# Performance work log

Hardware: AMD Instinct MI355X
Metric: run time of the kernel (lower is better)

Reference implementation:

```python
import jax, jax.numpy as jnp
import numpy as np

E = 1024
B = 16
SV = 576
SL = 448


def setup_inputs() -> dict:
    key = jax.random.key(0)
    k1, k2, k3, k4, k5 = jax.random.split(key, 5)
    return {
        "vision_tokens": jax.random.normal(k1, (B, SV, E), dtype=jnp.float32),
        "language_tokens": jax.random.normal(k2, (B, SL, E), dtype=jnp.float32),
        "Wv": jax.random.normal(k3, (E, E), dtype=jnp.float32) * 0.02,  # vision_proj.weight
        "Wl": jax.random.normal(k4, (E, E), dtype=jnp.float32) * 0.02,  # language_proj.weight
        "Wo": jax.random.normal(k5, (E, E), dtype=jnp.float32) * 0.02,  # out_proj.weight
        "bo": jnp.zeros((E,), dtype=jnp.float32),                        # out_proj.bias
    }


def reference(vision_tokens, language_tokens, Wv, Wl, Wo, bo):
    # Separate modality projections (nn.Linear, no bias): y = x @ W.T
    vp = jnp.einsum("bsd,ed->bse", vision_tokens, Wv)
    lp = jnp.einsum("bsd,ed->bse", language_tokens, Wl)
    # Concat vision+language tokens along sequence dim
    x = jnp.concatenate([vp, lp], axis=1)  # [B, SV+SL, E]
    scale = x.shape[-1] ** -0.5  # 1/sqrt(embed_dim), single-head as in CPU path
    scores = jnp.einsum("bqe,bke->bqk", x, x) * scale
    attn = jax.nn.softmax(scores, axis=-1)
    attended = jnp.einsum("bqk,bke->bqe", attn, x)
    # out_proj (with bias)
    return jnp.einsum("bse,fe->bsf", attended, Wo) + bo
```

## Files before the change

kernel.cpp:

```cpp
#include <hip/hip_runtime.h>

typedef _Float16 f16;
typedef _Float16 f16x4 __attribute__((ext_vector_type(4)));
typedef _Float16 f16x8 __attribute__((ext_vector_type(8)));
typedef float f32x4 __attribute__((ext_vector_type(4)));

#define AS1(p) ((const __attribute__((address_space(1))) void*)(p))
#define AS3(p) ((__attribute__((address_space(3))) void*)(p))
#define BAR() { asm volatile("" ::: "memory"); __builtin_amdgcn_s_barrier(); \
                asm volatile("" ::: "memory"); __builtin_amdgcn_sched_barrier(0); }
#define VMCNT(n) asm volatile("s_waitcnt vmcnt(" #n ")" ::: "memory")

__global__ void conv_all(const float* __restrict__ vis, const float* __restrict__ lan,
                         const float* __restrict__ Wv, const float* __restrict__ Wl,
                         const float* __restrict__ Wo,
                         f16* __restrict__ Ah, f16* __restrict__ Wh,
                         long nV4, long nL4, long nW4) {
  const long i = (long)blockIdx.x * blockDim.x + threadIdx.x;
  const float* src;
  f16* dst;
  long soff, doff;
  if (i < nV4) {
    const long perB = 576l * 256;
    long b = i / perB, off = i % perB;
    src = vis; soff = i;
    dst = Ah + b * 1048576; doff = off;
  } else if (i < nV4 + nL4) {
    long j = i - nV4;
    const long perB = 448l * 256;
    long b = j / perB, off = j % perB;
    src = lan; soff = j;
    dst = Ah + b * 1048576 + 576l * 1024; doff = off;
  } else {
    long j = i - nV4 - nL4;
    if (j >= 3 * nW4) return;
    long which = j / nW4, off = j % nW4;
    src = which == 0 ? Wv : (which == 1 ? Wl : Wo);
    soff = off;
    dst = Wh + which * 1048576; doff = off;
  }
  const float4 v = ((const float4*)src)[soff];
  f16x4 o = { (f16)v.x, (f16)v.y, (f16)v.z, (f16)v.w };
  ((f16x4*)dst)[doff] = o;
}

template<int OUTF>
__global__ __launch_bounds__(512, 2)
void gemm256(const f16* __restrict__ A, const f16* __restrict__ Bw,
             void* __restrict__ Cv, const float* __restrict__ bias,
             int M, long sA, long sB, long sC, float scale,
             int GX, int CHY, int NBYC, int CPG)
{
  constexpr int K = 1024, N = 1024, T = K / 64;
  __shared__ __align__(16) char lds[131072];

  const int id = blockIdx.x;
  const int xcd = id & 7, q = id >> 3;
  const int wi = q % CPG, ghi = q / CPG;
  const int g = xcd + 8 * ghi;
  const int bchunk = g % NBYC, bz = g / NBYC;
  const int bx = wi % GX, by = bchunk * CHY + wi / GX;

  const f16* Ab = A + (long)bz * sA;
  const f16* Bb = Bw + (long)bz * sB;
  const int t = threadIdx.x;
  const int w = t >> 6, l = t & 63;
  const int wr = w >> 2, wc = w & 3;
  const int brow = by * 256, bcol = bx * 256;

  f32x4 acc[2][4][2][2] = {};

  const int srow = t >> 3;
  const int scol = ((t & 7) * 8) ^ (((t >> 3) & 7) << 3);
  const int xm = (l & 7) << 4;
  const int lrow = l & 15, lslot = (l >> 4) * 16;

  auto stageA = [&](int kt, int h) {
    char* dst = lds + (kt & 1) * 65536 + h * 16384;
    #pragma unroll
    for (int j = 0; j < 2; ++j) {
      int ar = brow + h * 128 + j * 64 + srow;
      if (ar >= M) ar = M - 1;
      const f16* gp = Ab + (long)ar * K + kt * 64 + scol;
      __builtin_amdgcn_global_load_lds(AS1(gp), AS3(dst + j * 8192 + t * 16), 16, 0, 0);
    }
  };
  auto stageB = [&](int kt, int h) {
    char* dst = lds + (kt & 1) * 65536 + 32768 + h * 16384;
    #pragma unroll
    for (int j = 0; j < 2; ++j) {
      int br = bcol + h * 128 + j * 64 + srow;
      const f16* gp = Bb + (long)br * K + kt * 64 + scol;
      __builtin_amdgcn_global_load_lds(AS1(gp), AS3(dst + j * 8192 + t * 16), 16, 0, 0);
    }
  };
  auto ldA = [&](int kt, int mh, f16x8* a) {
    const char* base = lds + (kt & 1) * 65536;
    #pragma unroll
    for (int m4 = 0; m4 < 4; ++m4)
      #pragma unroll
      for (int kk = 0; kk < 2; ++kk) {
        int rowA = mh * 128 + wr * 64 + m4 * 16 + lrow;
        int off = (rowA * 128 + kk * 64 + lslot) ^ xm;
        a[m4 * 2 + kk] = *(const f16x8*)(base + off);
      }
  };
  auto ldB = [&](int kt, int nh, f16x8* b) {
    const char* base = lds + (kt & 1) * 65536 + 32768;
    #pragma unroll
    for (int n2 = 0; n2 < 2; ++n2)
      #pragma unroll
      for (int kk = 0; kk < 2; ++kk) {
        int rowB = nh * 128 + wc * 32 + n2 * 16 + lrow;
        int off = (rowB * 128 + kk * 64 + lslot) ^ xm;
        b[n2 * 2 + kk] = *(const f16x8*)(base + off);
      }
  };
  auto mma = [&](int mh, int nh, const f16x8* a, const f16x8* b) {
    __builtin_amdgcn_s_setprio(1);
    #pragma unroll
    for (int m4 = 0; m4 < 4; ++m4)
      #pragma unroll
      for (int n2 = 0; n2 < 2; ++n2)
        #pragma unroll
        for (int kk = 0; kk < 2; ++kk)
          acc[mh][m4][nh][n2] = __builtin_amdgcn_mfma_f32_16x16x32_f16(
              a[m4 * 2 + kk], b[n2 * 2 + kk], acc[mh][m4][nh][n2], 0, 0, 0);
    __builtin_amdgcn_s_setprio(0);
  };

  stageA(0, 0); stageA(0, 1); stageB(0, 0); stageB(0, 1);
  stageA(1, 0); stageB(1, 1);
  VMCNT(4);
  BAR();

  f16x8 a[8], b0[4], b1[4];
  for (int kt = 0; kt < T; ++kt) {
    ldA(kt, 0, a); ldB(kt, 0, b0);
    if (kt + 1 < T) stageA(kt + 1, 1);
    BAR();
    mma(0, 0, a, b0);
    BAR();
    ldB(kt, 1, b1);
    if (kt + 1 < T) stageB(kt + 1, 0);
    BAR();
    mma(0, 1, a, b1);
    BAR();
    ldA(kt, 1, a);
    if (kt + 2 < T) stageA(kt + 2, 0);
    BAR();
    mma(1, 1, a, b1);
    BAR();
    if (kt + 2 < T) {
      stageB(kt + 2, 1);
      VMCNT(4);
    } else if (kt + 1 < T) {
      VMCNT(0);
    }
    BAR();
    mma(1, 0, a, b0);
    BAR();
  }

  const int rj = (l >> 4) * 4;
  #pragma unroll
  for (int mh = 0; mh < 2; ++mh)
    #pragma unroll
    for (int m4 = 0; m4 < 4; ++m4)
      #pragma unroll
      for (int j = 0; j < 4; ++j) {
        const int r = brow + mh * 128 + wr * 64 + m4 * 16 + rj + j;
        if (r >= M) continue;
        #pragma unroll
        for (int nh = 0; nh < 2; ++nh)
          #pragma unroll
          for (int n2 = 0; n2 < 2; ++n2) {
            const int c = bcol + nh * 128 + wc * 32 + n2 * 16 + lrow;
            float v = acc[mh][m4][nh][n2][j];
            if constexpr (OUTF == 0) {
              ((f16*)Cv)[(long)bz * sC + (long)r * N + c] = (f16)v;
            } else if constexpr (OUTF == 1) {
              ((f16*)Cv)[(long)bz * sC + (long)r * N + c] = (f16)(v * scale);
            } else {
              ((float*)Cv)[(long)bz * sC + (long)r * N + c] = v + bias[c];
            }
          }
      }
}

__global__ __launch_bounds__(256)
void softmax_rows(f16* __restrict__ S) {
  const long row = blockIdx.x;
  f16* p = S + row * 1024;
  const int t = threadIdx.x;
  f16x4 v4 = ((f16x4*)p)[t];
  float v[4];
  #pragma unroll
  for (int j = 0; j < 4; ++j) v[j] = (float)v4[j];

  float m = fmaxf(fmaxf(v[0], v[1]), fmaxf(v[2], v[3]));
  #pragma unroll
  for (int off = 1; off < 64; off <<= 1) m = fmaxf(m, __shfl_xor(m, off));
  __shared__ float sm[4], ss[4];
  const int w = t >> 6;
  if ((t & 63) == 0) sm[w] = m;
  __syncthreads();
  m = fmaxf(fmaxf(sm[0], sm[1]), fmaxf(sm[2], sm[3]));

  float e[4], s = 0.f;
  #pragma unroll
  for (int j = 0; j < 4; ++j) { e[j] = __expf(v[j] - m); s += e[j]; }
  #pragma unroll
  for (int off = 1; off < 64; off <<= 1) s += __shfl_xor(s, off);
  if ((t & 63) == 0) ss[w] = s;
  __syncthreads();
  s = ss[0] + ss[1] + ss[2] + ss[3];
  const float inv = 1.f / s;

  f16x4 o;
  #pragma unroll
  for (int j = 0; j < 4; ++j) o[j] = (f16)(e[j] * inv);
  ((f16x4*)p)[t] = o;
}

__global__ __launch_bounds__(512)
void transpose_f16(const f16* __restrict__ in, f16* __restrict__ out) {
  __shared__ f16 tile[64][65];
  const long bs = (long)blockIdx.z * 1024 * 1024;
  const int r0 = blockIdx.y * 64, c0 = blockIdx.x * 64;
  const int tx = threadIdx.x, ty = threadIdx.y;
  #pragma unroll
  for (int i = 0; i < 8; ++i)
    tile[ty + 8 * i][tx] = in[bs + (long)(r0 + ty + 8 * i) * 1024 + c0 + tx];
  __syncthreads();
  #pragma unroll
  for (int i = 0; i < 8; ++i)
    out[bs + (long)(c0 + ty + 8 * i) * 1024 + r0 + tx] = tile[tx][ty + 8 * i];
}

extern "C" void kernel_launch(void* const* d_in, const int* in_sizes, int n_in,
                              void* d_out, int out_size, void* d_ws, size_t ws_size,
                              hipStream_t stream) {
  const float* vis = (const float*)d_in[0];
  const float* lan = (const float*)d_in[1];
  const float* Wv  = (const float*)d_in[2];
  const float* Wl  = (const float*)d_in[3];
  const float* Wo  = (const float*)d_in[4];
  const float* bo  = (const float*)d_in[5];
  float* out = (float*)d_out;

  const long PB = 1024l * 1024;
  const long SE = 16 * PB;

  f16* Ah  = (f16*)d_ws;
  f16* Xh  = Ah + SE;
  f16* Sc  = Xh + SE;
  f16* Wvh = Sc + SE;
  f16* Wlh = Wvh + PB;
  f16* Woh = Wlh + PB;
  f16* XhT = Ah;
  f16* Att = Xh;

  {
    const long nV4 = 16l * 576 * 1024 / 4;
    const long nL4 = 16l * 448 * 1024 / 4;
    const long nW4 = PB / 4;
    const long tot = nV4 + nL4 + 3 * nW4;
    conv_all<<<dim3((tot + 255) / 256), 256, 0, stream>>>(vis, lan, Wv, Wl, Wo,
                                                          Ah, Wvh, nV4, nL4, nW4);
  }
  gemm256<0><<<dim3(192), 512, 0, stream>>>(Ah, Wvh, Xh, nullptr, 576, PB, 0, PB, 1.f,
                                            4, 1, 3, 4);
  gemm256<0><<<dim3(128), 512, 0, stream>>>(Ah + 576l * 1024, Wlh, Xh + 576l * 1024,
                                            nullptr, 448, PB, 0, PB, 1.f,
                                            4, 1, 2, 4);
  gemm256<1><<<dim3(256), 512, 0, stream>>>(Xh, Xh, Sc, nullptr, 1024, PB, PB, PB,
                                            0.03125f, 4, 4, 1, 16);
  transpose_f16<<<dim3(16, 16, 16), dim3(64, 8), 0, stream>>>(Xh, XhT);
  softmax_rows<<<dim3(16 * 1024), 256, 0, stream>>>(Sc);
  gemm256<0><<<dim3(256), 512, 0, stream>>>(Sc, XhT, Att, nullptr, 1024, PB, PB, PB, 1.f,
                                            4, 4, 1, 16);
  gemm256<2><<<dim3(256), 512, 0, stream>>>(Att, Woh, out, bo, 16384, 0, 0, 0, 1.f,
                                            4, 8, 8, 32);
}
```

Before: 326.0 us.

## Template GEMM on M tile, split conversion kernels, single-wave softmax rows

Adds a BM template parameter to the GEMM so the language projection (448 rows) can use 128-row tiles, avoiding a padded 512-row tile at the cost of a second 256-block launch. Splits the fused fp32-to-fp16 conversion kernel into a token kernel with a 2D grid and a weight kernel, which removes 64-bit divides and modulos from the index math. Rewrites softmax to one 64-thread wave per row with 16 values per thread, dropping LDS and __syncthreads reductions. These three ideas are unrelated, and the extra launch and smaller tiles may reduce per-block efficiency.

Measured after the change: 318.7 us. 1.02x faster.

```diff
diff --git a/kernel.cpp b/kernel.cpp
--- a/kernel.cpp
+++ b/kernel.cpp
@@ -11,40 +11,31 @@
                 asm volatile("" ::: "memory"); __builtin_amdgcn_sched_barrier(0); }
 #define VMCNT(n) asm volatile("s_waitcnt vmcnt(" #n ")" ::: "memory")
 
-__global__ void conv_all(const float* __restrict__ vis, const float* __restrict__ lan,
-                         const float* __restrict__ Wv, const float* __restrict__ Wl,
-                         const float* __restrict__ Wo,
-                         f16* __restrict__ Ah, f16* __restrict__ Wh,
-                         long nV4, long nL4, long nW4) {
-  const long i = (long)blockIdx.x * blockDim.x + threadIdx.x;
-  const float* src;
-  f16* dst;
-  long soff, doff;
-  if (i < nV4) {
-    const long perB = 576l * 256;
-    long b = i / perB, off = i % perB;
-    src = vis; soff = i;
-    dst = Ah + b * 1048576; doff = off;
-  } else if (i < nV4 + nL4) {
-    long j = i - nV4;
-    const long perB = 448l * 256;
-    long b = j / perB, off = j % perB;
-    src = lan; soff = j;
-    dst = Ah + b * 1048576 + 576l * 1024; doff = off;
-  } else {
-    long j = i - nV4 - nL4;
-    if (j >= 3 * nW4) return;
-    long which = j / nW4, off = j % nW4;
-    src = which == 0 ? Wv : (which == 1 ? Wl : Wo);
-    soff = off;
-    dst = Wh + which * 1048576; doff = off;
-  }
-  const float4 v = ((const float4*)src)[soff];
+
+__global__ void conv_tokens2(const float* __restrict__ vis, const float* __restrict__ lan,
+                             f16* __restrict__ Ah) {
+  const int b = blockIdx.y;
+  const long i = (long)blockIdx.x * 256 + threadIdx.x;
+  const float4* src4 = (i < 147456)
+      ? (const float4*)vis + (long)b * 147456 + i
+      : (const float4*)lan + (long)b * 114688 + (i - 147456);
+  const float4 v = *src4;
   f16x4 o = { (f16)v.x, (f16)v.y, (f16)v.z, (f16)v.w };
-  ((f16x4*)dst)[doff] = o;
-}
-
-template<int OUTF>
+  ((f16x4*)Ah)[(long)b * 262144 + i] = o;
+}
+
+__global__ void conv_w3(const float* __restrict__ Wv, const float* __restrict__ Wl,
+                        const float* __restrict__ Wo, f16* __restrict__ Wh) {
+  const long i = (long)blockIdx.x * 256 + threadIdx.x;
+  const int which = (int)(i >> 18);
+  const long off = i & 262143;
+  const float* src = which == 0 ? Wv : (which == 1 ? Wl : Wo);
+  const float4 v = ((const float4*)src)[off];
+  f16x4 o = { (f16)v.x, (f16)v.y, (f16)v.z, (f16)v.w };
+  ((f16x4*)Wh)[i] = o;
+}
+
+template<int OUTF, int BM>
 __global__ __launch_bounds__(512, 2)
 void gemm256(const f16* __restrict__ A, const f16* __restrict__ Bw,
              void* __restrict__ Cv, const float* __restrict__ bias,
@@ -52,7 +43,11 @@
              int GX, int CHY, int NBYC, int CPG)
 {
   constexpr int K = 1024, N = 1024, T = K / 64;
-  __shared__ __align__(16) char lds[131072];
+  constexpr int AH = BM * 64;
+  constexpr int BUFSZ = 2 * AH + 32768;
+  constexpr int MR = BM / 64;
+  constexpr int AJ = BM / 128;
+  __shared__ __align__(16) char lds[2 * BUFSZ];
 
   const int id = blockIdx.x;
   const int xcd = id & 7, q = id >> 3;
@@ -66,9 +61,9 @@
   const int t = threadIdx.x;
   const int w = t >> 6, l = t & 63;
   const int wr = w >> 2, wc = w & 3;
-  const int brow = by * 256, bcol = bx * 256;
-
-  f32x4 acc[2][4][2][2] = {};
+  const int brow = by * BM, bcol = bx * 256;
+
+  f32x4 acc[2][MR][2][2] = {};
 
   const int srow = t >> 3;
   const int scol = ((t & 7) * 8) ^ (((t >> 3) & 7) << 3);
@@ -76,17 +71,17 @@
   const int lrow = l & 15, lslot = (l >> 4) * 16;
 
   auto stageA = [&](int kt, int h) {
-    char* dst = lds + (kt & 1) * 65536 + h * 16384;
-    #pragma unroll
-    for (int j = 0; j < 2; ++j) {
-      int ar = brow + h * 128 + j * 64 + srow;
+    char* dst = lds + (kt & 1) * BUFSZ + h * AH;
+    #pragma unroll
+    for (int j = 0; j < AJ; ++j) {
+      int ar = brow + h * (BM / 2) + j * 64 + srow;
       if (ar >= M) ar = M - 1;
       const f16* gp = Ab + (long)ar * K + kt * 64 + scol;
       __builtin_amdgcn_global_load_lds(AS1(gp), AS3(dst + j * 8192 + t * 16), 16, 0, 0);
     }
   };
   auto stageB = [&](int kt, int h) {
-    char* dst = lds + (kt & 1) * 65536 + 32768 + h * 16384;
+    char* dst = lds + (kt & 1) * BUFSZ + 2 * AH + h * 16384;
     #pragma unroll
     for (int j = 0; j < 2; ++j) {
       int br = bcol + h * 128 + j * 64 + srow;
@@ -95,18 +90,18 @@
     }
   };
   auto ldA = [&](int kt, int mh, f16x8* a) {
-    const char* base = lds + (kt & 1) * 65536;
-    #pragma unroll
-    for (int m4 = 0; m4 < 4; ++m4)
+    const char* base = lds + (kt & 1) * BUFSZ;
+    #pragma unroll
+    for (int m4 = 0; m4 < MR; ++m4)
       #pragma unroll
       for (int kk = 0; kk < 2; ++kk) {
-        int rowA = mh * 128 + wr * 64 + m4 * 16 + lrow;
+        int rowA = mh * (BM / 2) + wr * (BM / 4) + m4 * 16 + lrow;
         int off = (rowA * 128 + kk * 64 + lslot) ^ xm;
         a[m4 * 2 + kk] = *(const f16x8*)(base + off);
       }
   };
   auto ldB = [&](int kt, int nh, f16x8* b) {
-    const char* base = lds + (kt & 1) * 65536 + 32768;
+    const char* base = lds + (kt & 1) * BUFSZ + 2 * AH;
     #pragma unroll
     for (int n2 = 0; n2 < 2; ++n2)
       #pragma unroll
@@ -119,7 +114,7 @@
   auto mma = [&](int mh, int nh, const f16x8* a, const f16x8* b) {
     __builtin_amdgcn_s_setprio(1);
     #pragma unroll
-    for (int m4 = 0; m4 < 4; ++m4)
+    for (int m4 = 0; m4 < MR; ++m4)
       #pragma unroll
       for (int n2 = 0; n2 < 2; ++n2)
         #pragma unroll
@@ -131,10 +126,10 @@
 
   stageA(0, 0); stageA(0, 1); stageB(0, 0); stageB(0, 1);
   stageA(1, 0); stageB(1, 1);
-  VMCNT(4);
+  if constexpr (BM == 256) { VMCNT(4); } else { VMCNT(3); }
   BAR();
 
-  f16x8 a[8], b0[4], b1[4];
+  f16x8 a[2 * MR], b0[4], b1[4];
   for (int kt = 0; kt < T; ++kt) {
     ldA(kt, 0, a); ldB(kt, 0, b0);
     if (kt + 1 < T) stageA(kt + 1, 1);
@@ -153,7 +148,7 @@
     BAR();
     if (kt + 2 < T) {
       stageB(kt + 2, 1);
-      VMCNT(4);
+      if constexpr (BM == 256) { VMCNT(4); } else { VMCNT(3); }
     } else if (kt + 1 < T) {
       VMCNT(0);
     }
@@ -166,10 +161,10 @@
   #pragma unroll
   for (int mh = 0; mh < 2; ++mh)
     #pragma unroll
-    for (int m4 = 0; m4 < 4; ++m4)
+    for (int m4 = 0; m4 < MR; ++m4)
       #pragma unroll
       for (int j = 0; j < 4; ++j) {
-        const int r = brow + mh * 128 + wr * 64 + m4 * 16 + rj + j;
+        const int r = brow + mh * (BM / 2) + wr * (BM / 4) + m4 * 16 + rj + j;
         if (r >= M) continue;
         #pragma unroll
         for (int nh = 0; nh < 2; ++nh)
@@ -188,39 +183,33 @@
       }
 }
 
-__global__ __launch_bounds__(256)
+__global__ __launch_bounds__(64)
 void softmax_rows(f16* __restrict__ S) {
   const long row = blockIdx.x;
-  f16* p = S + row * 1024;
+  f16x8* p8 = (f16x8*)(S + row * 1024);
   const int t = threadIdx.x;
-  f16x4 v4 = ((f16x4*)p)[t];
-  float v[4];
-  #pragma unroll
-  for (int j = 0; j < 4; ++j) v[j] = (float)v4[j];
-
-  float m = fmaxf(fmaxf(v[0], v[1]), fmaxf(v[2], v[3]));
+  f16x8 va = p8[t], vb = p8[t + 64];
+  float v[16];
+  #pragma unroll
+  for (int j = 0; j < 8; ++j) { v[j] = (float)va[j]; v[8 + j] = (float)vb[j]; }
+
+  float m = v[0];
+  #pragma unroll
+  for (int j = 1; j < 16; ++j) m = fmaxf(m, v[j]);
   #pragma unroll
   for (int off = 1; off < 64; off <<= 1) m = fmaxf(m, __shfl_xor(m, off));
-  __shared__ float sm[4], ss[4];
-  const int w = t >> 6;
-  if ((t & 63) == 0) sm[w] = m;
-  __syncthreads();
-  m = fmaxf(fmaxf(sm[0], sm[1]), fmaxf(sm[2], sm[3]));
-
-  float e[4], s = 0.f;
-  #pragma unroll
-  for (int j = 0; j < 4; ++j) { e[j] = __expf(v[j] - m); s += e[j]; }
+
+  float s = 0.f;
+  #pragma unroll
+  for (int j = 0; j < 16; ++j) { v[j] = __expf(v[j] - m); s += v[j]; }
   #pragma unroll
   for (int off = 1; off < 64; off <<= 1) s += __shfl_xor(s, off);
-  if ((t & 63) == 0) ss[w] = s;
-  __syncthreads();
-  s = ss[0] + ss[1] + ss[2] + ss[3];
   const float inv = 1.f / s;
 
-  f16x4 o;
-  #pragma unroll
-  for (int j = 0; j < 4; ++j) o[j] = (f16)(e[j] * inv);
-  ((f16x4*)p)[t] = o;
+  f16x8 oa, ob;
+  #pragma unroll
+  for (int j = 0; j < 8; ++j) { oa[j] = (f16)(v[j] * inv); ob[j] = (f16)(v[8 + j] * inv); }
+  p8[t] = oa; p8[t + 64] = ob;
 }
 
 __global__ __launch_bounds__(512)
@@ -261,25 +250,20 @@
   f16* XhT = Ah;
   f16* Att = Xh;
 
-  {
-    const long nV4 = 16l * 576 * 1024 / 4;
-    const long nL4 = 16l * 448 * 1024 / 4;
-    const long nW4 = PB / 4;
-    const long tot = nV4 + nL4 + 3 * nW4;
-    conv_all<<<dim3((tot + 255) / 256), 256, 0, stream>>>(vis, lan, Wv, Wl, Wo,
-                                                          Ah, Wvh, nV4, nL4, nW4);
-  }
-  gemm256<0><<<dim3(192), 512, 0, stream>>>(Ah, Wvh, Xh, nullptr, 576, PB, 0, PB, 1.f,
-                                            4, 1, 3, 4);
-  gemm256<0><<<dim3(128), 512, 0, stream>>>(Ah + 576l * 1024, Wlh, Xh + 576l * 1024,
-                                            nullptr, 448, PB, 0, PB, 1.f,
-                                            4, 1, 2, 4);
-  gemm256<1><<<dim3(256), 512, 0, stream>>>(Xh, Xh, Sc, nullptr, 1024, PB, PB, PB,
-                                            0.03125f, 4, 4, 1, 16);
+  conv_tokens2<<<dim3(1024, 16), 256, 0, stream>>>(vis, lan, Ah);
+  conv_w3<<<dim3(3072), 256, 0, stream>>>(Wv, Wl, Wo, Wvh);
+
+  gemm256<0, 256><<<dim3(192), 512, 0, stream>>>(Ah, Wvh, Xh, nullptr, 576, PB, 0, PB, 1.f,
+                                                 4, 1, 3, 4);
+  gemm256<0, 128><<<dim3(256), 512, 0, stream>>>(Ah + 576l * 1024, Wlh, Xh + 576l * 1024,
+                                                 nullptr, 448, PB, 0, PB, 1.f,
+                                                 4, 1, 4, 4);
+  gemm256<1, 256><<<dim3(256), 512, 0, stream>>>(Xh, Xh, Sc, nullptr, 1024, PB, PB, PB,
+                                                 0.03125f, 4, 4, 1, 16);
   transpose_f16<<<dim3(16, 16, 16), dim3(64, 8), 0, stream>>>(Xh, XhT);
-  softmax_rows<<<dim3(16 * 1024), 256, 0, stream>>>(Sc);
-  gemm256<0><<<dim3(256), 512, 0, stream>>>(Sc, XhT, Att, nullptr, 1024, PB, PB, PB, 1.f,
-                                            4, 4, 1, 16);
-  gemm256<2><<<dim3(256), 512, 0, stream>>>(Att, Woh, out, bo, 16384, 0, 0, 0, 1.f,
-                                            4, 8, 8, 32);
-}
+  softmax_rows<<<dim3(16 * 1024), 64, 0, stream>>>(Sc);
+  gemm256<0, 256><<<dim3(256), 512, 0, stream>>>(Sc, XhT, Att, nullptr, 1024, PB, PB, PB, 1.f,
+                                                 4, 4, 1, 16);
+  gemm256<2, 256><<<dim3(256), 512, 0, stream>>>(Att, Woh, out, bo, 16384, 0, 0, 0, 1.f,
+                                                 4, 8, 8, 32);
+}
```
